# Kernel tuning notes

Hardware: AMD Instinct MI355X
Metric: run time of the kernel (lower is better)

## Reference

```python
import jax, jax.numpy as jnp
import numpy as np

B, S, D = 16, 512, 512
H, HS, HSEL = 8, 2, 2      # heads, shared heads, selected routed heads
NB = 2                     # num_block -> L = 3*NB layers (NB knowledge + 2*NB question)
L = 3 * NB
DFF = 2048


def setup_inputs() -> dict:
    key = jax.random.key(0)
    ks = jax.random.split(key, 12)
    s = 0.02
    return {
        'question_emb': jax.random.normal(ks[0], (B, S, D), jnp.float32),
        'interaction_emb': jax.random.normal(ks[1], (B, S, D), jnp.float32),
        'wq': jax.random.normal(ks[2], (L, D, D), jnp.float32) * s,
        'bq': jnp.zeros((L, D), jnp.float32),
        'wv': jax.random.normal(ks[3], (L, D, D), jnp.float32) * s,
        'bv': jnp.zeros((L, D), jnp.float32),
        'wo': jax.random.normal(ks[4], (L, D, D), jnp.float32) * s,
        'bo': jnp.zeros((L, D), jnp.float32),
        'wg': jax.random.normal(ks[5], (L, D, H - HS), jnp.float32) * s,
        'ln1_g': jnp.ones((L, D), jnp.float32),
        'ln1_b': jnp.zeros((L, D), jnp.float32),
        'fw1': jax.random.normal(ks[6], (L, D, DFF), jnp.float32) * s,
        'fb1': jnp.zeros((L, DFF), jnp.float32),
        'fw2': jax.random.normal(ks[7], (L, DFF, D), jnp.float32) * s,
        'fb2': jnp.zeros((L, D), jnp.float32),
        'ln2_g': jnp.ones((L, D), jnp.float32),
        'ln2_b': jnp.zeros((L, D), jnp.float32),
    }


def _ln(x, g, b, eps=1e-5):
    mu = x.mean(-1, keepdims=True)
    var = ((x - mu) ** 2).mean(-1, keepdims=True)
    return g * (x - mu) / jnp.sqrt(var + eps) + b


def _forward(question_emb, interaction_emb, wq, bq, wv, bv, wo, bo, wg,
             ln1_g, ln1_b, fw1, fb1, fw2, fb2, ln2_g, ln2_b):
    def block(x_q, x_v, i, mask_flag, apply_pos):
        b, s, d = x_q.shape
        dk = d // H
        # mask_flag=True -> allow j<=i (strict future masked); False -> allow j<i
        allowed = jnp.tril(jnp.ones((s, s), bool), 0 if mask_flag else -1)
        qlin = x_q @ wq[i] + bq[i]                                   # kq_same: k = q
        v = (x_v @ wv[i] + bv[i]).reshape(b, s, H, dk).transpose(0, 2, 1, 3)
        qh = qlin.reshape(b, s, H, dk).transpose(0, 2, 1, 3)         # [b,h,s,dk]
        scores = jnp.einsum('bhqd,bhkd->bhqk', qh, qh) / jnp.sqrt(jnp.float32(dk))
        scores = jnp.where(allowed[None, None], scores, jnp.float32(-1e9))
        scores = scores.at[:, :, 0, :].set(0.0)                      # pad_zero row 0
        # dynamic head routing over non-shared heads
        gates = jax.nn.softmax((qlin @ wg[i]).reshape(b * s, H - HS), axis=-1)
        _, idx = jax.lax.top_k(gates, HSEL)
        dmask = jnp.zeros_like(gates).at[jnp.arange(b * s)[:, None], idx].set(1.0)
        dyn = (gates * dmask).reshape(b, s, H - HS)
        rmask = jnp.concatenate([jnp.ones((b, s, HS), gates.dtype), dyn], axis=-1)
        rmask = rmask.mean(axis=1)                                   # [b,H]
        attn = jax.nn.softmax(scores, axis=-1)
        ctx = jnp.einsum('bhqk,bhkd->bhqd', attn, v) * rmask[:, :, None, None]
        ctx = ctx.transpose(0, 2, 1, 3).reshape(b, s, d)
        x = _ln(x_q + ctx @ wo[i] + bo[i], ln1_g[i], ln1_b[i])
        if apply_pos:
            ffn = jax.nn.relu(x @ fw1[i] + fb1[i]) @ fw2[i] + fb2[i]
            x = _ln(x + ffn, ln2_g[i], ln2_b[i])
        return x

    y = interaction_emb
    for i in range(NB):                 # knowledge encoder
        y = block(y, y, i, True, False)
    x = question_emb
    li = NB
    for j in range(2 * NB):             # question encoder, alternating
        if j % 2 == 0:
            x = block(x, x, li, True, False)
        else:
            x = block(x, y, li, False, True)
        li += 1
    return x


def reference(question_emb, interaction_emb, wq, bq, wv, bv, wo, bo, wg,
              ln1_g, ln1_b, fw1, fb1, fw2, fb2, ln2_g, ln2_b):
    return _forward(question_emb, interaction_emb, wq, bq, wv, bv, wo, bo, wg,
                    ln1_g, ln1_b, fw1, fb1, fw2, fb2, ln2_g, ln2_b)
```

## Files before the change

### kernel.cpp

```cpp
#include <hip/hip_runtime.h>
#include <hip/hip_bf16.h>

#define BSZ 16
#define SEQ 512
#define DIM 512
#define NH 8
#define DK 64
#define NROWS (BSZ*SEQ)
#define DFF2 2048

typedef unsigned short u16;
typedef u16   u16x8 __attribute__((ext_vector_type(8)));
typedef short s16x8 __attribute__((ext_vector_type(8)));
typedef float f32x4 __attribute__((ext_vector_type(4)));

__device__ __forceinline__ u16 f2b(float x) {
    union { float f; unsigned int u; } c; c.f = x;
    unsigned int r = c.u + 0x7fff + ((c.u >> 16) & 1);
    return (u16)(r >> 16);
}
__device__ __forceinline__ float b2f(u16 u) {
    union { unsigned int i; float f; } c; c.i = ((unsigned int)u) << 16; return c.f;
}

__device__ __forceinline__ void gld16(const u16* g, u16* l) {
    __builtin_amdgcn_global_load_lds(
        (const __attribute__((address_space(1))) unsigned int*)(unsigned long long)g,
        (__attribute__((address_space(3))) unsigned int*)(unsigned int)(unsigned long long)l,
        16, 0, 0);
}

__global__ __launch_bounds__(256) void cast_f2b4(const float* __restrict__ in,
                                                 u16* __restrict__ out, int n4) {
    int i = blockIdx.x * 256 + threadIdx.x;
    if (i >= n4) return;
    float4 v = ((const float4*)in)[i];
    ushort4 o; o.x = f2b(v.x); o.y = f2b(v.y); o.z = f2b(v.z); o.w = f2b(v.w);
    ((ushort4*)out)[i] = o;
}

__global__ __launch_bounds__(256) void transpose_cast(
    const float* __restrict__ W, u16* __restrict__ WT,
    int K, int N, int layer0, int lstride, size_t dstride)
{
    __shared__ float t[32][33];
    int z = blockIdx.z;
    const float* Wz = W + (size_t)(layer0 + z * lstride) * K * N;
    u16* WTz = WT + (size_t)z * dstride;
    int k0 = blockIdx.x * 32, n0 = blockIdx.y * 32;
    int tx = threadIdx.x & 31, ty = threadIdx.x >> 5;
    for (int i = ty; i < 32; i += 8) t[i][tx] = Wz[(size_t)(k0 + i) * N + n0 + tx];
    __syncthreads();
    for (int i = ty; i < 32; i += 8) WTz[(size_t)(n0 + i) * K + k0 + tx] = f2b(t[tx][i]);
}

template<int WRITE_BF16, int RELU, int ACCUM, int SPLIT>
__global__ __launch_bounds__(256) void gemm2(
    const u16* __restrict__ Aq, const u16* __restrict__ Av,
    const u16* __restrict__ WT,
    const float* __restrict__ bias1, const float* __restrict__ bias2,
    void* __restrict__ C1, void* __restrict__ C2,
    int K, int lda, int ldw, int ldc, int nsplit, int nx)
{
    __shared__ __attribute__((aligned(16))) u16 As[2][128 * 32];
    __shared__ __attribute__((aligned(16))) u16 Bs[2][128 * 32];
    int tid = threadIdx.x;
    int wave = tid >> 6, lane = tid & 63;
    int quad = lane >> 4, l16 = lane & 15;

    int bid = blockIdx.x;
    int per = gridDim.x >> 3;
    int swz = (bid & 7) * per + (bid >> 3);
    int bx = swz % nx, by = swz / nx;
    int n0 = bx * 128, m0 = by * 128;

    int wrow = (wave & 1) * 64, wcol = (wave >> 1) * 64;
    bool isv = SPLIT && (n0 >= nsplit);
    const u16* A = isv ? Av : Aq;

    int sr = wave * 32 + (lane >> 2);
    int sc = (lane & 3) * 8;
    const u16* gA0 = A  + (size_t)(m0 + sr) * lda + sc;
    const u16* gA1 = gA0 + (size_t)16 * lda;
    const u16* gB0 = WT + (size_t)(n0 + sr) * ldw + sc;
    const u16* gB1 = gB0 + (size_t)16 * ldw;
    int lo0 = (wave * 32) * 32;
    int lo1 = (wave * 32 + 16) * 32;

    f32x4 acc[4][4];
    #pragma unroll
    for (int i = 0; i < 4; i++)
        #pragma unroll
        for (int j = 0; j < 4; j++) acc[i][j] = (f32x4){0.f, 0.f, 0.f, 0.f};

    gld16(gA0, &As[0][lo0]);
    gld16(gA1, &As[0][lo1]);
    gld16(gB0, &Bs[0][lo0]);
    gld16(gB1, &Bs[0][lo1]);
    __syncthreads();

    int NT = K >> 5;
    int cur = 0;
    for (int t = 0; t < NT; ++t) {
        if (t + 1 < NT) {
            int k0 = (t + 1) << 5;
            gld16(gA0 + k0, &As[cur ^ 1][lo0]);
            gld16(gA1 + k0, &As[cur ^ 1][lo1]);
            gld16(gB0 + k0, &Bs[cur ^ 1][lo0]);
            gld16(gB1 + k0, &Bs[cur ^ 1][lo1]);
        }
        s16x8 af[4], bf[4];
        #pragma unroll
        for (int i = 0; i < 4; i++) {
            af[i] = *(s16x8*)&As[cur][(wrow + i * 16 + l16) * 32 + quad * 8];
            bf[i] = *(s16x8*)&Bs[cur][(wcol + i * 16 + l16) * 32 + quad * 8];
        }
        #pragma unroll
        for (int mi = 0; mi < 4; mi++)
            #pragma unroll
            for (int ni = 0; ni < 4; ni++)
                acc[mi][ni] = __builtin_amdgcn_mfma_f32_16x16x32_bf16(
                    af[mi], bf[ni], acc[mi][ni], 0, 0, 0);
        __syncthreads();
        cur ^= 1;
    }

    const float* bias = isv ? bias2 : bias1;
    void* C = isv ? C2 : C1;
    int nb = n0 - (isv ? nsplit : 0);
    #pragma unroll
    for (int ni = 0; ni < 4; ni++) {
        int cn = nb + wcol + ni * 16 + l16;
        float bb = bias ? bias[cn] : 0.f;
        #pragma unroll
        for (int mi = 0; mi < 4; mi++) {
            int cm = m0 + wrow + mi * 16 + quad * 4;
            #pragma unroll
            for (int r = 0; r < 4; r++) {
                size_t off = (size_t)(cm + r) * ldc + cn;
                float v = acc[mi][ni][r] + bb;
                if (ACCUM) v += ((float*)C)[off];
                if (RELU) v = fmaxf(v, 0.f);
                if (WRITE_BF16) ((u16*)C)[off] = f2b(v);
                else            ((float*)C)[off] = v;
            }
        }
    }
}

__global__ void init_rmask6(float* __restrict__ r) {
    int t = blockIdx.x * 256 + threadIdx.x;
    if (t < 6 * 128) r[t] = ((t & 7) < 2) ? 1.0f : 0.0f;
}

__global__ __launch_bounds__(256) void router_kernel(
    const u16* __restrict__ qlin, const float* __restrict__ wg,
    float* __restrict__ rmask)
{
    __shared__ float s_wg[6 * 544];
    __shared__ float sacc[8];
    int tid = threadIdx.x;
    #pragma unroll
    for (int k = 0; k < 12; k++) {
        int n = tid + k * 256;
        int d = n / 6, r = n - d * 6;
        s_wg[r * 544 + (d >> 4) * 17 + (d & 15)] = wg[n];
    }
    if (tid < 8) sacc[tid] = 0.f;
    __syncthreads();

    int c = tid & 31;
    int row = blockIdx.x * 8 + (tid >> 5);
    int cb = c * 17;
    const u16* xr = qlin + (size_t)row * DIM + c * 16;
    u16x8 q0 = *(const u16x8*)xr;
    u16x8 q1 = *(const u16x8*)(xr + 8);

    float lg[6] = {0.f, 0.f, 0.f, 0.f, 0.f, 0.f};
    #pragma unroll
    for (int j = 0; j < 8; j++) {
        float x = b2f(q0[j]);
        #pragma unroll
        for (int r = 0; r < 6; r++) lg[r] += x * s_wg[r * 544 + cb + j];
    }
    #pragma unroll
    for (int j = 0; j < 8; j++) {
        float x = b2f(q1[j]);
        #pragma unroll
        for (int r = 0; r < 6; r++) lg[r] += x * s_wg[r * 544 + cb + 8 + j];
    }
    #pragma unroll
    for (int r = 0; r < 6; r++) {
        #pragma unroll
        for (int o = 1; o < 32; o <<= 1) lg[r] += __shfl_xor(lg[r], o);
    }
    float m = lg[0];
    #pragma unroll
    for (int r = 1; r < 6; r++) m = fmaxf(m, lg[r]);
    float s = 0.f;
    #pragma unroll
    for (int r = 0; r < 6; r++) { lg[r] = __expf(lg[r] - m); s += lg[r]; }
    float inv = 1.0f / s;
    #pragma unroll
    for (int r = 0; r < 6; r++) lg[r] *= inv;
    int i1 = 0; float g1 = lg[0];
    #pragma unroll
    for (int r = 1; r < 6; r++) if (lg[r] > g1) { g1 = lg[r]; i1 = r; }
    int i2 = -1; float g2 = -1.f;
    #pragma unroll
    for (int r = 0; r < 6; r++) if (r != i1 && lg[r] > g2) { g2 = lg[r]; i2 = r; }
    if (c == 0) {
        atomicAdd(&sacc[i1], g1);
        atomicAdd(&sacc[i2], g2);
    }
    __syncthreads();
    if (tid < 6) {
        int b = blockIdx.x >> 6;
        atomicAdd(&rmask[b * 8 + 2 + tid], sacc[tid] * (1.0f / (float)SEQ));
    }
}

__global__ __launch_bounds__(256) void transpose_v(
    const u16* __restrict__ v, u16* __restrict__ vT)
{
    __shared__ u16 t[64][72];
    int jt = blockIdx.x, bh = blockIdx.y;
    int b = bh >> 3, h = bh & 7;
    int tid = threadIdx.x;
    int lr = tid >> 2, lc = (tid & 3) * 16;
    const u16* src = v + (size_t)(b * SEQ + jt * 64 + lr) * DIM + h * DK + lc;
    *(u16x8*)&t[lr][lc]     = *(const u16x8*)src;
    *(u16x8*)&t[lr][lc + 8] = *(const u16x8*)(src + 8);
    __syncthreads();
    u16x8 o0, o1;
    #pragma unroll
    for (int i = 0; i < 8; i++) o0[i] = t[lc + i][lr];
    #pragma unroll
    for (int i = 0; i < 8; i++) o1[i] = t[lc + 8 + i][lr];
    u16* dst = vT + ((size_t)bh * DK + lr) * SEQ + jt * 64 + lc;
    *(u16x8*)dst       = o0;
    *(u16x8*)(dst + 8) = o1;
}

__global__ __launch_bounds__(256) void attn_flash(
    const u16* __restrict__ qlin, const u16* __restrict__ vT,
    const float* __restrict__ rmask, u16* __restrict__ ctx, int mask_flag)
{
    __shared__ u16 s_q [64][72];
    __shared__ u16 s_k [64][72];
    __shared__ u16 s_vt[64][72];
    __shared__ u16 s_p [64][72];
    int qt = blockIdx.x, h = blockIdx.y, b = blockIdx.z;
    int tid = threadIdx.x;
    int wave = tid >> 6, lane = tid & 63;
    int quad = lane >> 4, l16 = lane & 15;
    int lr = tid >> 2, lc = (tid & 3) * 16;

    {
        const u16* src = qlin + (size_t)(b * SEQ + qt * 64 + lr) * DIM + h * DK + lc;
        *(u16x8*)&s_q[lr][lc]     = *(const u16x8*)src;
        *(u16x8*)&s_q[lr][lc + 8] = *(const u16x8*)(src + 8);
    }

    f32x4 acc_o[4];
    #pragma unroll
    for (int i = 0; i < 4; i++) acc_o[i] = (f32x4){0.f, 0.f, 0.f, 0.f};
    float m_i[4] = {-1e30f, -1e30f, -1e30f, -1e30f};
    float l_i[4] = {0.f, 0.f, 0.f, 0.f};

    for (int jt = 0; jt <= qt; jt++) {
        const u16* ksrc = qlin + (size_t)(b * SEQ + jt * 64 + lr) * DIM + h * DK + lc;
        const u16* vtsrc = vT + ((size_t)(b * NH + h) * DK + lr) * SEQ + jt * 64 + lc;
        u16x8 k0 = *(const u16x8*)ksrc,  k1 = *(const u16x8*)(ksrc + 8);
        u16x8 v0 = *(const u16x8*)vtsrc, v1 = *(const u16x8*)(vtsrc + 8);
        __syncthreads();
        *(u16x8*)&s_k[lr][lc]      = k0;
        *(u16x8*)&s_k[lr][lc + 8]  = k1;
        *(u16x8*)&s_vt[lr][lc]     = v0;
        *(u16x8*)&s_vt[lr][lc + 8] = v1;
        __syncthreads();

        f32x4 acc_s[4];
        #pragma unroll
        for (int i = 0; i < 4; i++) acc_s[i] = (f32x4){0.f, 0.f, 0.f, 0.f};
        #pragma unroll
        for (int ks = 0; ks < 2; ks++) {
            s16x8 a = *(s16x8*)&s_q[wave * 16 + l16][ks * 32 + quad * 8];
            #pragma unroll
            for (int nf = 0; nf < 4; nf++) {
                s16x8 bb = *(s16x8*)&s_k[nf * 16 + l16][ks * 32 + quad * 8];
                acc_s[nf] = __builtin_amdgcn_mfma_f32_16x16x32_bf16(a, bb, acc_s[nf], 0, 0, 0);
            }
        }

        int qg0 = qt * 64 + wave * 16 + quad * 4;
        float sc[4][4];
        #pragma unroll
        for (int nf = 0; nf < 4; nf++) {
            int jg = jt * 64 + nf * 16 + l16;
            #pragma unroll
            for (int r = 0; r < 4; r++) {
                float v = acc_s[nf][r] * 0.125f;
                if (jt == qt) {
                    int bound = mask_flag ? (qg0 + r) : (qg0 + r - 1);
                    if (jg > bound) v = -1e30f;
                }
                sc[nf][r] = v;
            }
        }
        float tmax[4];
        #pragma unroll
        for (int r = 0; r < 4; r++) {
            float t = fmaxf(fmaxf(sc[0][r], sc[1][r]), fmaxf(sc[2][r], sc[3][r]));
            #pragma unroll
            for (int o = 1; o < 16; o <<= 1) t = fmaxf(t, __shfl_xor(t, o));
            tmax[r] = t;
        }
        float p[4][4];
        #pragma unroll
        for (int r = 0; r < 4; r++) {
            float mnew = fmaxf(m_i[r], tmax[r]);
            float alpha = __expf(m_i[r] - mnew);
            float su = 0.f;
            #pragma unroll
            for (int nf = 0; nf < 4; nf++) { p[nf][r] = __expf(sc[nf][r] - mnew); su += p[nf][r]; }
            #pragma unroll
            for (int o = 1; o < 16; o <<= 1) su += __shfl_xor(su, o);
            l_i[r] = l_i[r] * alpha + su;
            m_i[r] = mnew;
            #pragma unroll
            for (int nf = 0; nf < 4; nf++) acc_o[nf][r] *= alpha;
        }
        #pragma unroll
        for (int nf = 0; nf < 4; nf++)
            #pragma unroll
            for (int r = 0; r < 4; r++)
                s_p[wave * 16 + quad * 4 + r][nf * 16 + l16] = f2b(p[nf][r]);

        #pragma unroll
        for (int ks = 0; ks < 2; ks++) {
            s16x8 a = *(s16x8*)&s_p[wave * 16 + l16][ks * 32 + quad * 8];
            #pragma unroll
            for (int nf = 0; nf < 4; nf++) {
                s16x8 bb = *(s16x8*)&s_vt[nf * 16 + l16][ks * 32 + quad * 8];
                acc_o[nf] = __builtin_amdgcn_mfma_f32_16x16x32_bf16(a, bb, acc_o[nf], 0, 0, 0);
            }
        }
    }

    float rm = rmask[b * 8 + h];
    int qrow = qt * 64 + wave * 16 + quad * 4;
    #pragma unroll
    for (int r = 0; r < 4; r++) {
        float scale = rm / l_i[r];
        u16* dst = ctx + (size_t)(b * SEQ + qrow + r) * DIM + h * DK;
        #pragma unroll
        for (int nf = 0; nf < 4; nf++)
            dst[nf * 16 + l16] = f2b(acc_o[nf][r] * scale);
    }
}

__global__ __launch_bounds__(256) void attn_row0(
    const u16* __restrict__ vT, const float* __restrict__ rmask, u16* __restrict__ ctx)
{
    int bh = blockIdx.x;
    int b = bh >> 3, h = bh & 7;
    int d = threadIdx.x >> 2, seg = threadIdx.x & 3;
    const u16* src = vT + ((size_t)bh * DK + d) * SEQ + seg * 128;
    float s = 0.f;
    for (int i = 0; i < 16; i++) {
        u16x8 v = *(const u16x8*)(src + i * 8);
        #pragma unroll
        for (int j = 0; j < 8; j++) s += b2f(v[j]);
    }
    s += __shfl_down(s, 1);
    s += __shfl_down(s, 2);
    if (seg == 0)
        ctx[(size_t)(b * SEQ) * DIM + h * DK + d] =
            f2b(s * (1.0f / (float)SEQ) * rmask[b * 8 + h]);
}

__global__ __launch_bounds__(256) void add_ln_c(
    float* __restrict__ x, const float* __restrict__ y,
    const float* __restrict__ g, const float* __restrict__ bta,
    u16* __restrict__ out16)
{
    __shared__ float redA[4], redB[4];
    int row = blockIdx.x, tid = threadIdx.x;
    size_t base = (size_t)row * DIM;
    float t0 = x[base + tid] + y[base + tid];
    float t1 = x[base + tid + 256] + y[base + tid + 256];
    float s = t0 + t1, sq = t0 * t0 + t1 * t1;
    for (int o = 32; o > 0; o >>= 1) { s += __shfl_down(s, o, 64); sq += __shfl_down(sq, o, 64); }
    int lane = tid & 63, wid = tid >> 6;
    if (lane == 0) { redA[wid] = s; redB[wid] = sq; }
    __syncthreads();
    float S1 = redA[0] + redA[1] + redA[2] + redA[3];
    float S2 = redB[0] + redB[1] + redB[2] + redB[3];
    float mu = S1 * (1.0f / (float)DIM);
    float var = S2 * (1.0f / (float)DIM) - mu * mu;
    float rstd = rsqrtf(var + 1e-5f);
    float o0 = g[tid]       * (t0 - mu) * rstd + bta[tid];
    float o1 = g[tid + 256] * (t1 - mu) * rstd + bta[tid + 256];
    x[base + tid]       = o0;
    x[base + tid + 256] = o1;
    out16[base + tid]       = f2b(o0);
    out16[base + tid + 256] = f2b(o1);
}

extern "C" void kernel_launch(void* const* d_in, const int* in_sizes, int n_in,
                              void* d_out, int out_size, void* d_ws, size_t ws_size,
                              hipStream_t stream) {
    const float* qe   = (const float*)d_in[0];
    const float* ie   = (const float*)d_in[1];
    const float* wq   = (const float*)d_in[2];
    const float* bq   = (const float*)d_in[3];
    const float* wv   = (const float*)d_in[4];
    const float* bv   = (const float*)d_in[5];
    const float* wo   = (const float*)d_in[6];
    const float* bo   = (const float*)d_in[7];
    const float* wg   = (const float*)d_in[8];
    const float* ln1g = (const float*)d_in[9];
    const float* ln1b = (const float*)d_in[10];
    const float* fw1  = (const float*)d_in[11];
    const float* fb1  = (const float*)d_in[12];
    const float* fw2  = (const float*)d_in[13];
    const float* fb2  = (const float*)d_in[14];
    const float* ln2g = (const float*)d_in[15];
    const float* ln2b = (const float*)d_in[16];

    const size_t RD = (size_t)NROWS * DIM;
    float* ws   = (float*)d_ws;
    float* xbuf = ws;
    float* ybuf = ws + RD;

    u16* b16    = (u16*)(ws + 2 * RD);
    u16* x16    = b16;                 b16 += RD;
    u16* y16    = b16;                 b16 += RD;
    u16* ctx16  = b16;                 b16 += RD;
    u16* qlin16 = b16;                 b16 += RD;
    u16* vbuf16 = b16;                 b16 += RD;
    u16* vT     = b16;                 b16 += RD;
    u16* hid    = ctx16;
    float* proj = (float*)vbuf16;
    u16* wqvT   = b16;                 b16 += 6 * (size_t)1024 * 512;
    u16* woT    = b16;                 b16 += 6 * (size_t)512 * 512;
    u16* fw1T   = b16;                 b16 += 2 * (size_t)DFF2 * 512;
    u16* fw2T   = b16;                 b16 += 2 * (size_t)512 * DFF2;
    float* rmask6 = (float*)b16;

    const size_t nBytes = RD * sizeof(float);
    hipMemcpyAsync(xbuf, qe, nBytes, hipMemcpyDeviceToDevice, stream);
    hipMemcpyAsync(ybuf, ie, nBytes, hipMemcpyDeviceToDevice, stream);
    cast_f2b4<<<(int)(RD / 4 / 256), 256, 0, stream>>>(qe, x16, (int)(RD / 4));
    cast_f2b4<<<(int)(RD / 4 / 256), 256, 0, stream>>>(ie, y16, (int)(RD / 4));

    transpose_cast<<<dim3(16, 16, 6), 256, 0, stream>>>(wq, wqvT,             512, 512, 0, 1, (size_t)1024 * 512);
    transpose_cast<<<dim3(16, 16, 6), 256, 0, stream>>>(wv, wqvT + 512 * 512, 512, 512, 0, 1, (size_t)1024 * 512);
    transpose_cast<<<dim3(16, 16, 6), 256, 0, stream>>>(wo, woT,              512, 512, 0, 1, (size_t)512 * 512);
    transpose_cast<<<dim3(16, 64, 2), 256, 0, stream>>>(fw1, fw1T, 512, DFF2, 3, 2, (size_t)DFF2 * 512);
    transpose_cast<<<dim3(64, 16, 2), 256, 0, stream>>>(fw2, fw2T, DFF2, 512, 3, 2, (size_t)512 * DFF2);
    init_rmask6<<<3, 256, 0, stream>>>(rmask6);

    const int BIG = 1 << 30;
    auto run_block = [&](float* xr, u16* xq16, const u16* xv16, int l, int maskf, int pos) {
        size_t lD = (size_t)l * DIM;
        float* rm = rmask6 + l * 128;
        gemm2<1, 0, 0, 1><<<8 * 64, 256, 0, stream>>>(
            xq16, xv16, wqvT + (size_t)l * 1024 * 512, bq + lD, bv + lD,
            qlin16, vbuf16, 512, 512, 512, 512, 512, 8);
        transpose_v<<<dim3(8, 128), 256, 0, stream>>>(vbuf16, vT);
        router_kernel<<<NROWS / 8, 256, 0, stream>>>(qlin16, wg + (size_t)l * DIM * 6, rm);
        attn_flash<<<dim3(SEQ / 64, NH, BSZ), 256, 0, stream>>>(qlin16, vT, rm, ctx16, maskf);
        attn_row0<<<128, 256, 0, stream>>>(vT, rm, ctx16);
        gemm2<0, 0, 0, 0><<<4 * 64, 256, 0, stream>>>(
            ctx16, ctx16, woT + (size_t)l * 512 * 512, bo + lD, nullptr,
            proj, nullptr, 512, 512, 512, 512, BIG, 4);
        add_ln_c<<<NROWS, 256, 0, stream>>>(xr, proj, ln1g + lD, ln1b + lD, xq16);
        if (pos) {
            int slot = (l - 3) / 2;
            for (int c = 0; c < 2; c++) {
                gemm2<1, 1, 0, 0><<<8 * 64, 256, 0, stream>>>(
                    xq16, xq16,
                    fw1T + (size_t)slot * DFF2 * 512 + (size_t)c * 1024 * 512,
                    fb1 + (size_t)l * DFF2 + c * 1024, nullptr,
                    hid, nullptr, 512, 512, 512, 1024, BIG, 8);
                if (c == 0)
                    gemm2<0, 0, 0, 0><<<4 * 64, 256, 0, stream>>>(
                        hid, hid, fw2T + (size_t)slot * 512 * DFF2,
                        fb2 + lD, nullptr, proj, nullptr, 1024, 1024, DFF2, 512, BIG, 4);
                else
                    gemm2<0, 0, 1, 0><<<4 * 64, 256, 0, stream>>>(
                        hid, hid, fw2T + (size_t)slot * 512 * DFF2 + 1024,
                        nullptr, nullptr, proj, nullptr, 1024, 1024, DFF2, 512, BIG, 4);
            }
            add_ln_c<<<NROWS, 256, 0, stream>>>(xr, proj, ln2g + lD, ln2b + lD, xq16);
        }
    };

    run_block(ybuf, y16, y16, 0, 1, 0);
    run_block(ybuf, y16, y16, 1, 1, 0);
    run_block(xbuf, x16, x16, 2, 1, 0);
    run_block(xbuf, x16, y16, 3, 0, 1);
    run_block(xbuf, x16, x16, 4, 1, 0);
    run_block(xbuf, x16, y16, 5, 0, 1);

    hipMemcpyAsync(d_out, xbuf, nBytes, hipMemcpyDeviceToDevice, stream);
}
```

Baseline: 972.7 us.

## Use narrower GEMM tiles and split-K with fused partial-sum reduction in LayerNorm

The GEMM kernel gains a configurable tile width (NI=2 gives 128x64 tiles) and an optional two-way split-K mode that writes the two partial products to separate fp32 buffers. The output and FFN2 projections now use split-K, and the new add_ln2 kernel sums both partials plus the bias during the residual LayerNorm. The FFN1 GEMM now runs as a single launch over the full 2048-wide hidden layer instead of two chunks, using a larger dedicated hidden buffer. The goal is more workgroups per launch to fill the GPU's compute units and fewer launches and read-modify-write passes, at the cost of extra workspace and partial-sum memory traffic.

```diff
diff --git a/kernel.cpp b/kernel.cpp
--- a/kernel.cpp
+++ b/kernel.cpp
@@ -54,7 +54,7 @@
     for (int i = ty; i < 32; i += 8) WTz[(size_t)(n0 + i) * K + k0 + tx] = f2b(t[tx][i]);
 }
 
-template<int WRITE_BF16, int RELU, int ACCUM, int SPLIT>
+template<int WRITE_BF16, int RELU, int SPLIT, int SPLITK, int NI>
 __global__ __launch_bounds__(256) void gemm2(
     const u16* __restrict__ Aq, const u16* __restrict__ Av,
     const u16* __restrict__ WT,
@@ -63,7 +63,7 @@
     int K, int lda, int ldw, int ldc, int nsplit, int nx)
 {
     __shared__ __attribute__((aligned(16))) u16 As[2][128 * 32];
-    __shared__ __attribute__((aligned(16))) u16 Bs[2][128 * 32];
+    __shared__ __attribute__((aligned(16))) u16 Bs[2][NI * 32 * 32];
     int tid = threadIdx.x;
     int wave = tid >> 6, lane = tid & 63;
     int quad = lane >> 4, l16 = lane & 15;
@@ -71,32 +71,47 @@
     int bid = blockIdx.x;
     int per = gridDim.x >> 3;
     int swz = (bid & 7) * per + (bid >> 3);
+    int nxy = SPLITK ? ((int)gridDim.x >> 1) : (int)gridDim.x;
+    int kslice = 0;
+    if (SPLITK && swz >= nxy) { kslice = 1; swz -= nxy; }
     int bx = swz % nx, by = swz / nx;
-    int n0 = bx * 128, m0 = by * 128;
-
-    int wrow = (wave & 1) * 64, wcol = (wave >> 1) * 64;
+    int n0 = bx * (NI * 32), m0 = by * 128;
+
+    int wrow = (wave & 1) * 64;
+    int wcol = (wave >> 1) * (NI * 16);
     bool isv = SPLIT && (n0 >= nsplit);
     const u16* A = isv ? Av : Aq;
 
     int sr = wave * 32 + (lane >> 2);
     int sc = (lane & 3) * 8;
-    const u16* gA0 = A  + (size_t)(m0 + sr) * lda + sc;
+    int ko = kslice * K;
+    const u16* gA0 = A  + (size_t)(m0 + sr) * lda + sc + ko;
     const u16* gA1 = gA0 + (size_t)16 * lda;
-    const u16* gB0 = WT + (size_t)(n0 + sr) * ldw + sc;
-    const u16* gB1 = gB0 + (size_t)16 * ldw;
     int lo0 = (wave * 32) * 32;
     int lo1 = (wave * 32 + 16) * 32;
 
-    f32x4 acc[4][4];
+    const u16* gB0;
+    const u16* gB1 = nullptr;
+    int bo0, bo1 = 0;
+    if (NI == 4) {
+        gB0 = WT + (size_t)(n0 + sr) * ldw + sc + ko;
+        gB1 = gB0 + (size_t)16 * ldw;
+        bo0 = lo0; bo1 = lo1;
+    } else {
+        gB0 = WT + (size_t)(n0 + wave * 16 + (lane >> 2)) * ldw + sc + ko;
+        bo0 = (wave * 16) * 32;
+    }
+
+    f32x4 acc[4][NI];
     #pragma unroll
     for (int i = 0; i < 4; i++)
         #pragma unroll
-        for (int j = 0; j < 4; j++) acc[i][j] = (f32x4){0.f, 0.f, 0.f, 0.f};
+        for (int j = 0; j < NI; j++) acc[i][j] = (f32x4){0.f, 0.f, 0.f, 0.f};
 
     gld16(gA0, &As[0][lo0]);
     gld16(gA1, &As[0][lo1]);
-    gld16(gB0, &Bs[0][lo0]);
-    gld16(gB1, &Bs[0][lo1]);
+    gld16(gB0, &Bs[0][bo0]);
+    if (NI == 4) gld16(gB1, &Bs[0][bo1]);
     __syncthreads();
 
     int NT = K >> 5;
@@ -106,19 +121,20 @@
             int k0 = (t + 1) << 5;
             gld16(gA0 + k0, &As[cur ^ 1][lo0]);
             gld16(gA1 + k0, &As[cur ^ 1][lo1]);
-            gld16(gB0 + k0, &Bs[cur ^ 1][lo0]);
-            gld16(gB1 + k0, &Bs[cur ^ 1][lo1]);
-        }
-        s16x8 af[4], bf[4];
-        #pragma unroll
-        for (int i = 0; i < 4; i++) {
+            gld16(gB0 + k0, &Bs[cur ^ 1][bo0]);
+            if (NI == 4) gld16(gB1 + k0, &Bs[cur ^ 1][bo1]);
+        }
+        s16x8 af[4], bf[NI];
+        #pragma unroll
+        for (int i = 0; i < 4; i++)
             af[i] = *(s16x8*)&As[cur][(wrow + i * 16 + l16) * 32 + quad * 8];
+        #pragma unroll
+        for (int i = 0; i < NI; i++)
             bf[i] = *(s16x8*)&Bs[cur][(wcol + i * 16 + l16) * 32 + quad * 8];
-        }
         #pragma unroll
         for (int mi = 0; mi < 4; mi++)
             #pragma unroll
-            for (int ni = 0; ni < 4; ni++)
+            for (int ni = 0; ni < NI; ni++)
                 acc[mi][ni] = __builtin_amdgcn_mfma_f32_16x16x32_bf16(
                     af[mi], bf[ni], acc[mi][ni], 0, 0, 0);
         __syncthreads();
@@ -126,10 +142,10 @@
     }
 
     const float* bias = isv ? bias2 : bias1;
-    void* C = isv ? C2 : C1;
+    void* C = (isv || (SPLITK && kslice)) ? C2 : C1;
     int nb = n0 - (isv ? nsplit : 0);
     #pragma unroll
-    for (int ni = 0; ni < 4; ni++) {
+    for (int ni = 0; ni < NI; ni++) {
         int cn = nb + wcol + ni * 16 + l16;
         float bb = bias ? bias[cn] : 0.f;
         #pragma unroll
@@ -139,7 +155,6 @@
             for (int r = 0; r < 4; r++) {
                 size_t off = (size_t)(cm + r) * ldc + cn;
                 float v = acc[mi][ni][r] + bb;
-                if (ACCUM) v += ((float*)C)[off];
                 if (RELU) v = fmaxf(v, 0.f);
                 if (WRITE_BF16) ((u16*)C)[off] = f2b(v);
                 else            ((float*)C)[off] = v;
@@ -380,16 +395,17 @@
             f2b(s * (1.0f / (float)SEQ) * rmask[b * 8 + h]);
 }
 
-__global__ __launch_bounds__(256) void add_ln_c(
-    float* __restrict__ x, const float* __restrict__ y,
+__global__ __launch_bounds__(256) void add_ln2(
+    float* __restrict__ x, const float* __restrict__ p0, const float* __restrict__ p1,
+    const float* __restrict__ bcol,
     const float* __restrict__ g, const float* __restrict__ bta,
     u16* __restrict__ out16)
 {
     __shared__ float redA[4], redB[4];
     int row = blockIdx.x, tid = threadIdx.x;
     size_t base = (size_t)row * DIM;
-    float t0 = x[base + tid] + y[base + tid];
-    float t1 = x[base + tid + 256] + y[base + tid + 256];
+    float t0 = x[base + tid]       + p0[base + tid]       + p1[base + tid]       + bcol[tid];
+    float t1 = x[base + tid + 256] + p0[base + tid + 256] + p1[base + tid + 256] + bcol[tid + 256];
     float s = t0 + t1, sq = t0 * t0 + t1 * t1;
     for (int o = 32; o > 0; o >>= 1) { s += __shfl_down(s, o, 64); sq += __shfl_down(sq, o, 64); }
     int lane = tid & 63, wid = tid >> 6;
@@ -441,8 +457,9 @@
     u16* qlin16 = b16;                 b16 += RD;
     u16* vbuf16 = b16;                 b16 += RD;
     u16* vT     = b16;                 b16 += RD;
-    u16* hid    = ctx16;
-    float* proj = (float*)vbuf16;
+    float* proj0 = (float*)vbuf16;
+    u16* hid    = b16;                 b16 += 4 * RD;
+    float* proj1 = (float*)b16;        b16 += 2 * RD;
     u16* wqvT   = b16;                 b16 += 6 * (size_t)1024 * 512;
     u16* woT    = b16;                 b16 += 6 * (size_t)512 * 512;
     u16* fw1T   = b16;                 b16 += 2 * (size_t)DFF2 * 512;
@@ -466,35 +483,29 @@
     auto run_block = [&](float* xr, u16* xq16, const u16* xv16, int l, int maskf, int pos) {
         size_t lD = (size_t)l * DIM;
         float* rm = rmask6 + l * 128;
-        gemm2<1, 0, 0, 1><<<8 * 64, 256, 0, stream>>>(
+        gemm2<1, 0, 1, 0, 2><<<1024, 256, 0, stream>>>(
             xq16, xv16, wqvT + (size_t)l * 1024 * 512, bq + lD, bv + lD,
-            qlin16, vbuf16, 512, 512, 512, 512, 512, 8);
+            qlin16, vbuf16, 512, 512, 512, 512, 512, 16);
         transpose_v<<<dim3(8, 128), 256, 0, stream>>>(vbuf16, vT);
         router_kernel<<<NROWS / 8, 256, 0, stream>>>(qlin16, wg + (size_t)l * DIM * 6, rm);
         attn_flash<<<dim3(SEQ / 64, NH, BSZ), 256, 0, stream>>>(qlin16, vT, rm, ctx16, maskf);
         attn_row0<<<128, 256, 0, stream>>>(vT, rm, ctx16);
-        gemm2<0, 0, 0, 0><<<4 * 64, 256, 0, stream>>>(
-            ctx16, ctx16, woT + (size_t)l * 512 * 512, bo + lD, nullptr,
-            proj, nullptr, 512, 512, 512, 512, BIG, 4);
-        add_ln_c<<<NROWS, 256, 0, stream>>>(xr, proj, ln1g + lD, ln1b + lD, xq16);
+        gemm2<0, 0, 0, 1, 2><<<1024, 256, 0, stream>>>(
+            ctx16, ctx16, woT + (size_t)l * 512 * 512, nullptr, nullptr,
+            proj0, proj1, 256, 512, 512, 512, BIG, 8);
+        add_ln2<<<NROWS, 256, 0, stream>>>(xr, proj0, proj1, bo + lD,
+                                           ln1g + lD, ln1b + lD, xq16);
         if (pos) {
             int slot = (l - 3) / 2;
-            for (int c = 0; c < 2; c++) {
-                gemm2<1, 1, 0, 0><<<8 * 64, 256, 0, stream>>>(
-                    xq16, xq16,
-                    fw1T + (size_t)slot * DFF2 * 512 + (size_t)c * 1024 * 512,
-                    fb1 + (size_t)l * DFF2 + c * 1024, nullptr,
-                    hid, nullptr, 512, 512, 512, 1024, BIG, 8);
-                if (c == 0)
-                    gemm2<0, 0, 0, 0><<<4 * 64, 256, 0, stream>>>(
-                        hid, hid, fw2T + (size_t)slot * 512 * DFF2,
-                        fb2 + lD, nullptr, proj, nullptr, 1024, 1024, DFF2, 512, BIG, 4);
-                else
-                    gemm2<0, 0, 1, 0><<<4 * 64, 256, 0, stream>>>(
-                        hid, hid, fw2T + (size_t)slot * 512 * DFF2 + 1024,
-                        nullptr, nullptr, proj, nullptr, 1024, 1024, DFF2, 512, BIG, 4);
-            }
-            add_ln_c<<<NROWS, 256, 0, stream>>>(xr, proj, ln2g + lD, ln2b + lD, xq16);
+            gemm2<1, 1, 0, 0, 2><<<2048, 256, 0, stream>>>(
+                xq16, xq16, fw1T + (size_t)slot * DFF2 * 512,
+                fb1 + (size_t)l * DFF2, nullptr,
+                hid, nullptr, 512, 512, 512, DFF2, BIG, 32);
+            gemm2<0, 0, 0, 1, 2><<<1024, 256, 0, stream>>>(
+                hid, hid, fw2T + (size_t)slot * 512 * DFF2, nullptr, nullptr,
+                proj0, proj1, 1024, DFF2, DFF2, 512, BIG, 8);
+            add_ln2<<<NROWS, 256, 0, stream>>>(xr, proj0, proj1, fb2 + lD,
+                                               ln2g + lD, ln2b + lD, xq16);
         }
     };
 
```

After: 925.4 us. 4.9% less time.
